# Kernel optimization log

Hardware: AMD Instinct MI355X
Metric: run time of the kernel (lower is better)

The kernel has to match this reference:

```python
import jax, jax.numpy as jnp
import numpy as np

D_MODEL, D_STATE, D_CONV, EXPAND = 384, 16, 4, 2
D_INNER = EXPAND * D_MODEL          # 768
DT_RANK = (D_MODEL + 15) // 16      # 24
BATCH, SEQ = 4, 1024


def setup_inputs() -> dict:
    key = jax.random.key(0)
    ks = jax.random.split(key, 16)
    s = 0.02
    inp = {
        "x": jax.random.normal(ks[0], (BATCH, SEQ, D_MODEL), jnp.float32),
        # LayerNorm
        "ln_g": jnp.ones((D_MODEL,), jnp.float32),
        "ln_b": jnp.zeros((D_MODEL,), jnp.float32),
        # in_proj: d_model -> 2*d_model
        "W_in": jax.random.normal(ks[1], (D_MODEL, 2 * D_MODEL), jnp.float32) * s,
        "b_in": jnp.zeros((2 * D_MODEL,), jnp.float32),
        # SSM: input projection d_model -> d_inner
        "W_si": jax.random.normal(ks[2], (D_MODEL, D_INNER), jnp.float32) * s,
        "b_si": jnp.zeros((D_INNER,), jnp.float32),
        # depthwise causal conv (d_inner, 1, d_conv)
        "conv_w": jax.random.normal(ks[3], (D_INNER, 1, D_CONV), jnp.float32) * s,
        "conv_b": jnp.zeros((D_INNER,), jnp.float32),
        # x_proj: d_inner -> dt_rank + 2*d_state (no bias)
        "W_x": jax.random.normal(ks[4], (D_INNER, DT_RANK + 2 * D_STATE), jnp.float32) * s,
        # dt_proj: dt_rank -> d_inner
        "W_dt": jax.random.normal(ks[5], (DT_RANK, D_INNER), jnp.float32) * s,
        "b_dt": jnp.full((D_INNER,), -4.6, jnp.float32),  # softplus(-4.6) ~ 0.01
        # S4D-real init: A = -exp(A_log)
        "A_log": jnp.broadcast_to(jnp.log(jnp.arange(1, D_STATE + 1, dtype=jnp.float32)), (D_INNER, D_STATE)).copy(),
        "D_skip": jnp.ones((D_INNER,), jnp.float32),
        # SSM output projection d_inner -> d_model
        "W_so": jax.random.normal(ks[6], (D_INNER, D_MODEL), jnp.float32) * s,
        "b_so": jnp.zeros((D_MODEL,), jnp.float32),
        # block out_proj
        "W_out": jax.random.normal(ks[7], (D_MODEL, D_MODEL), jnp.float32) * s,
        "b_out": jnp.zeros((D_MODEL,), jnp.float32),
    }
    return inp


def _silu(v):
    return v * jax.nn.sigmoid(v)


def _selective_ssm(xb, W_si, b_si, conv_w, conv_b, W_x, W_dt, b_dt, A_log, D_skip, W_so, b_so):
    # xb: (B, L, d_model) -> (B, L, d_model)
    u = xb @ W_si + b_si                              # (B,L,Di)
    # causal depthwise conv over L
    uc = jax.lax.conv_general_dilated(
        u.transpose(0, 2, 1), conv_w,
        window_strides=(1,), padding=[(D_CONV - 1, 0)],
        feature_group_count=D_INNER,
        dimension_numbers=("NCH", "OIH", "NCH"))
    u = _silu(uc.transpose(0, 2, 1) + conv_b)          # (B,L,Di)

    x_dbl = u @ W_x                                    # (B,L,dt_rank+2N)
    dtr = x_dbl[..., :DT_RANK]
    Bm = x_dbl[..., DT_RANK:DT_RANK + D_STATE]         # (B,L,N)
    Cm = x_dbl[..., DT_RANK + D_STATE:]                # (B,L,N)
    dt = jax.nn.softplus(dtr @ W_dt + b_dt)            # (B,L,Di)

    A = -jnp.exp(A_log)                                # (Di,N)
    dA = jnp.exp(dt[..., None] * A)                    # (B,L,Di,N)
    dBu = dt[..., None] * Bm[:, :, None, :] * u[..., None]  # (B,L,Di,N)

    def step(h, ts):
        dA_t, dBu_t, C_t = ts                          # (B,Di,N),(B,Di,N),(B,N)
        h = dA_t * h + dBu_t
        y = jnp.einsum("bdn,bn->bd", h, C_t)
        return h, y

    h0 = jnp.zeros((u.shape[0], D_INNER, D_STATE), u.dtype)
    _, ys = jax.lax.scan(step, h0,
                         (dA.transpose(1, 0, 2, 3), dBu.transpose(1, 0, 2, 3), Cm.transpose(1, 0, 2)))
    y = ys.transpose(1, 0, 2) + u * D_skip             # (B,L,Di)
    return y @ W_so + b_so                             # (B,L,d_model)


def reference(x, ln_g, ln_b, W_in, b_in, W_si, b_si, conv_w, conv_b, W_x, W_dt, b_dt,
              A_log, D_skip, W_so, b_so, W_out, b_out):
    residual = x
    mu = jnp.mean(x, axis=-1, keepdims=True)
    var = jnp.var(x, axis=-1, keepdims=True)
    xn = (x - mu) * jax.lax.rsqrt(var + 1e-5) * ln_g + ln_b
    xz = xn @ W_in + b_in
    xb, zb = jnp.split(xz, 2, axis=-1)                 # each (B,L,d_model)

    ssm = lambda v: _selective_ssm(v, W_si, b_si, conv_w, conv_b, W_x, W_dt, b_dt,
                                   A_log, D_skip, W_so, b_so)
    h_fwd = ssm(xb)
    h_bwd = jnp.flip(ssm(jnp.flip(xb, axis=1)), axis=1)

    y = (h_fwd + h_bwd) * _silu(zb)
    out = y @ W_out + b_out
    return residual + out
```

## Files before the change

### kernel.cpp

```cpp
#include <hip/hip_runtime.h>


#define SEQ   1024
#define BATCH 4
#define DM    384
#define DI    768
#define DS    16
#define DTRK  24
#define NX    56
#define ROWS  (BATCH*SEQ)
#define NC    64
#define TC    (SEQ/NC)

#define LOG2E 1.4426950408889634f
#define LN2   0.6931471805599453f

typedef __bf16 bf16;
typedef __attribute__((ext_vector_type(8))) __bf16 bf16x8;
typedef __attribute__((ext_vector_type(4))) float f32x4;

__device__ __forceinline__ float fast_silu(float z) {
    return z * __builtin_amdgcn_rcpf(1.f + __builtin_exp2f(-z * LOG2E));
}
__device__ __forceinline__ float fast_softplus(float v) {
    return (v > 20.f) ? v : __builtin_log2f(1.f + __builtin_exp2f(v * LOG2E)) * LN2;
}

__global__ __launch_bounds__(64) void ln_kernel(
    const float* __restrict__ x, const float* __restrict__ g,
    const float* __restrict__ b, bf16* __restrict__ xn)
{
    int row = blockIdx.x;
    int lane = threadIdx.x;
    const float* xr = x + (size_t)row * DM;
    float v[6]; float s = 0.f, s2 = 0.f;
#pragma unroll
    for (int i = 0; i < 6; ++i) { v[i] = xr[lane + i*64]; s += v[i]; s2 += v[i]*v[i]; }
#pragma unroll
    for (int off = 32; off > 0; off >>= 1) { s += __shfl_down(s, off); s2 += __shfl_down(s2, off); }
    s = __shfl(s, 0); s2 = __shfl(s2, 0);
    float mu = s * (1.f/DM);
    float var = s2 * (1.f/DM) - mu*mu;
    float rs = rsqrtf(var + 1e-5f);
    bf16* xo = xn + (size_t)row * DM;
#pragma unroll
    for (int i = 0; i < 6; ++i) { int c = lane + i*64; xo[c] = (bf16)((v[i]-mu)*rs*g[c] + b[c]); }
}

#define WPE0 294912
#define WPE1 589824
#define WPE2 632832
#define WPE3 927744
#define WPE4 1075200
#define WPTOT (WPE4 + DI*64)
__global__ __launch_bounds__(256) void wprep_kernel(
    const float* __restrict__ W_in, const float* __restrict__ W_si,
    const float* __restrict__ W_x,  const float* __restrict__ W_so,
    const float* __restrict__ W_out, const float* __restrict__ W_dt,
    bf16* __restrict__ wt)
{
    int i = blockIdx.x*256 + threadIdx.x;
    if (i >= WPTOT) return;
    if (i >= WPE4) {
        int j = i - WPE4;
        int n = j >> 6, k = j & 63;
        wt[i] = (k < DTRK) ? (bf16)W_dt[(size_t)k*DI + n] : (bf16)0.f;
        return;
    }
    const float* W; int K, N, base;
    if (i < WPE0)      { W = W_in;  K = 384; N = 768; base = 0; }
    else if (i < WPE1) { W = W_si;  K = 384; N = 768; base = WPE0; }
    else if (i < WPE2) { W = W_x;   K = 768; N = 56;  base = WPE1; }
    else if (i < WPE3) { W = W_so;  K = 768; N = 384; base = WPE2; }
    else               { W = W_out; K = 384; N = 384; base = WPE3; }
    int j = i - base;
    int n = j / K, k = j % K;
    wt[i] = (bf16)W[(size_t)k*N + n];
}

template<int BN>
__global__ __launch_bounds__(256) void gemm_mfma(
    const bf16* __restrict__ A, const bf16* __restrict__ A2, int lda,
    const bf16* __restrict__ Bt,
    const float* __restrict__ bias, float bias_scale,
    float* __restrict__ Cf, int ldcf, int ncut,
    bf16* __restrict__ Cb, int ldcb,
    int M, int N, int K,
    int epi, const float* __restrict__ eptr, int lde)
{
    __shared__ bf16 As[64][72];
    __shared__ bf16 Bs[BN][72];
    const int tid = threadIdx.x;

    int bx = blockIdx.x, by = blockIdx.y;
    {
        int nbx = gridDim.x, nby = gridDim.y;
        if ((nby & 7) == 0) {
            int id = by * nbx + bx;
            int xcd = id & 7, rest = id >> 3;
            int mPerX = nby >> 3;
            by = xcd * mPerX + rest / nbx;
            bx = rest % nbx;
        }
    }
    const int n0 = bx * BN;
    const int m0 = by * 64;
    const int l = tid & 63, w = tid >> 6;
    const int wm = (w >> 1) * 32;
    const int wn = (BN == 64) ? (w & 1) * 32 : (w & 1) * 16;
    const int lm = l & 15, kg = l >> 4;

    const int ar = tid >> 2;
    const int ak = (tid & 3) * 16;

    f32x4 acc[2][BN == 64 ? 2 : 1];
#pragma unroll
    for (int i = 0; i < 2; ++i)
#pragma unroll
        for (int j = 0; j < (BN == 64 ? 2 : 1); ++j) acc[i][j] = (f32x4){0.f,0.f,0.f,0.f};

    for (int k0 = 0; k0 < K; k0 += 64) {
        {
            const bf16* Ab = A + (size_t)(m0+ar)*lda + k0 + ak;
            bf16x8 v0 = *(const bf16x8*)(Ab);
            bf16x8 v1 = *(const bf16x8*)(Ab+8);
            if (A2) {
                const bf16* Ab2 = A2 + (size_t)(m0+ar)*lda + k0 + ak;
                bf16x8 u0 = *(const bf16x8*)(Ab2);
                bf16x8 u1 = *(const bf16x8*)(Ab2+8);
#pragma unroll
                for (int e = 0; e < 8; ++e) {
                    v0[e] = (bf16)((float)v0[e] + (float)u0[e]);
                    v1[e] = (bf16)((float)v1[e] + (float)u1[e]);
                }
            }
            *(bf16x8*)&As[ar][ak]   = v0;
            *(bf16x8*)&As[ar][ak+8] = v1;
        }
        if (BN == 64) {
            int bn = tid >> 2, bk = (tid & 3) * 16;
            int gn = n0 + bn;
            if (gn < N) {
                const bf16* Bp = Bt + (size_t)gn*K + k0 + bk;
                bf16x8 b0 = *(const bf16x8*)(Bp);
                bf16x8 b1 = *(const bf16x8*)(Bp+8);
                *(bf16x8*)&Bs[bn][bk]   = b0;
                *(bf16x8*)&Bs[bn][bk+8] = b1;
            } else {
                bf16x8 z = {};
                *(bf16x8*)&Bs[bn][bk]   = z;
                *(bf16x8*)&Bs[bn][bk+8] = z;
            }
        } else {
            int bn = tid >> 3, bk = (tid & 7) * 8;
            int gn = n0 + bn;
            if (gn < N) {
                *(bf16x8*)&Bs[bn][bk] = *(const bf16x8*)(Bt + (size_t)gn*K + k0 + bk);
            } else {
                bf16x8 z = {};
                *(bf16x8*)&Bs[bn][bk] = z;
            }
        }
        __syncthreads();
#pragma unroll
        for (int kk = 0; kk < 2; ++kk) {
            int co = kk*32 + kg*8;
            bf16x8 a0 = *(const bf16x8*)&As[wm +  0 + lm][co];
            bf16x8 a1 = *(const bf16x8*)&As[wm + 16 + lm][co];
            bf16x8 b0 = *(const bf16x8*)&Bs[wn +  0 + lm][co];
            acc[0][0] = __builtin_amdgcn_mfma_f32_16x16x32_bf16(a0, b0, acc[0][0], 0, 0, 0);
            acc[1][0] = __builtin_amdgcn_mfma_f32_16x16x32_bf16(a1, b0, acc[1][0], 0, 0, 0);
            if (BN == 64) {
                bf16x8 b1 = *(const bf16x8*)&Bs[wn + 16 + lm][co];
                acc[0][BN==64?1:0] = __builtin_amdgcn_mfma_f32_16x16x32_bf16(a0, b1, acc[0][BN==64?1:0], 0, 0, 0);
                acc[1][BN==64?1:0] = __builtin_amdgcn_mfma_f32_16x16x32_bf16(a1, b1, acc[1][BN==64?1:0], 0, 0, 0);
            }
        }
        __syncthreads();
    }

    constexpr int NT = (BN == 64) ? 2 : 1;
    int r0 = kg * 4;
#pragma unroll
    for (int mt = 0; mt < 2; ++mt) {
        int mbase = m0 + wm + mt*16 + r0;
#pragma unroll
        for (int nt = 0; nt < NT; ++nt) {
            int n = n0 + wn + nt*16 + lm;
            if (n >= N) continue;
            float bv = bias ? bias_scale * bias[n] : 0.f;
#pragma unroll
            for (int r = 0; r < 4; ++r) {
                int mm = mbase + r;
                float v = acc[mt][nt][r] + bv;
                if (epi == 1) {
                    v = fast_softplus(v);
                } else if (epi == 2) {
                    v *= fast_silu(eptr[(size_t)mm*lde + n]);
                } else if (epi == 3) {
                    v += eptr[(size_t)mm*lde + n];
                }
                if (Cb) Cb[(size_t)mm*ldcb + n] = (bf16)v;
                if (Cf && n >= ncut) Cf[(size_t)mm*ldcf + (n - ncut)] = v;
            }
        }
    }
}

__global__ __launch_bounds__(256) void conv_silu_kernel(
    const bf16* __restrict__ up, const float* __restrict__ w,
    const float* __restrict__ cb, bf16* __restrict__ uf_bf, bf16* __restrict__ ub_bf)
{
    int i = blockIdx.x * 256 + threadIdx.x;
    if (i >= ROWS*DI) return;
    int d = i % DI;
    int row = i / DI;
    int t = row % SEQ;
    float w0 = w[d*4+0], w1 = w[d*4+1], w2 = w[d*4+2], w3 = w[d*4+3];
    float bias = cb[d];
    const bf16* col = up + (size_t)(row - t) * DI + d;

    float af = bias + (float)col[(size_t)t*DI] * w3;
    if (t >= 1) af += (float)col[(size_t)(t-1)*DI] * w2;
    if (t >= 2) af += (float)col[(size_t)(t-2)*DI] * w1;
    if (t >= 3) af += (float)col[(size_t)(t-3)*DI] * w0;

    float ab = bias + (float)col[(size_t)t*DI] * w3;
    if (t+1 < SEQ) ab += (float)col[(size_t)(t+1)*DI] * w2;
    if (t+2 < SEQ) ab += (float)col[(size_t)(t+2)*DI] * w1;
    if (t+3 < SEQ) ab += (float)col[(size_t)(t+3)*DI] * w0;

    uf_bf[i] = (bf16)fast_silu(af);
    ub_bf[i] = (bf16)fast_silu(ab);
}


__global__ __launch_bounds__(256) void scan_phase_a(
    const bf16* __restrict__ dt, const bf16* __restrict__ u,
    const float* __restrict__ xbc, const float* __restrict__ A_log,
    float* __restrict__ hend, float* __restrict__ sumdt)
{
    int blk = blockIdx.x;
    int dgrp = blk % 3;
    int c = (blk / 3) % NC;
    int dirb = blk / (3*NC);
    int dir = dirb >> 2, b = dirb & 3;
    int d = dgrp * 256 + threadIdx.x;

    size_t base  = ((size_t)dir*ROWS + (size_t)b*SEQ) * DI;
    size_t xbase = ((size_t)dir*ROWS + (size_t)b*SEQ) * 32;

    float c1 = -expf(A_log[d*DS]) * LOG2E;
    float h[DS];
#pragma unroll
    for (int n = 0; n < DS; ++n) h[n] = 0.f;
    float sdt = 0.f;

    for (int s = c*TC; s < (c+1)*TC; ++s) {
        int t = dir ? (SEQ-1-s) : s;
        size_t row = base + (size_t)t * DI;
        float dtv = (float)dt[row + d];
        float uv  = (float)u[row + d];
        sdt += dtv;
        const float* xr = xbc + xbase + (size_t)t * 32;
        float dtu = dtv * uv;
        float r = __builtin_exp2f(dtv * c1);
        float p = 1.f;
#pragma unroll
        for (int n = 0; n < DS; ++n) {
            p *= r;
            h[n] = p * h[n] + xr[n] * dtu;
        }
    }
    size_t cb = (size_t)dirb*NC + c;
    sumdt[cb*DI + d] = sdt;
#pragma unroll
    for (int n = 0; n < DS; ++n)
        hend[(cb*DS + n)*DI + d] = h[n];
}

__global__ __launch_bounds__(256) void scan_phase_b(
    const float* __restrict__ A_log, const float* __restrict__ sumdt,
    float* __restrict__ hstate)
{
    int dirb = blockIdx.x / 48;
    int pair = (blockIdx.x % 48) * 256 + threadIdx.x;
    int n = pair / DI;
    int d = pair % DI;
    float Ac = -expf(A_log[d*DS + n]) * LOG2E;
    float H = 0.f;
    for (int c = 0; c < NC; ++c) {
        size_t cb = (size_t)dirb*NC + c;
        float sdt = sumdt[cb*DI + d];
        size_t idx = (cb*DS + n)*DI + d;
        float he = hstate[idx];
        hstate[idx] = H;
        H = __builtin_exp2f(Ac * sdt) * H + he;
    }
}

__global__ __launch_bounds__(256) void scan_phase_c(
    const bf16* __restrict__ dt, const bf16* __restrict__ u,
    const float* __restrict__ xbc, const float* __restrict__ A_log,
    const float* __restrict__ D_skip, const float* __restrict__ h0,
    bf16* __restrict__ ys)
{
    int blk = blockIdx.x;
    int dgrp = blk % 3;
    int c = (blk / 3) % NC;
    int dirb = blk / (3*NC);
    int dir = dirb >> 2, b = dirb & 3;
    int d = dgrp * 256 + threadIdx.x;

    size_t base  = ((size_t)dir*ROWS + (size_t)b*SEQ) * DI;
    size_t xbase = ((size_t)dir*ROWS + (size_t)b*SEQ) * 32;

    float c1 = -expf(A_log[d*DS]) * LOG2E;
    float h[DS];
    size_t cb = (size_t)dirb*NC + c;
#pragma unroll
    for (int n = 0; n < DS; ++n) h[n] = h0[(cb*DS + n)*DI + d];
    float Dv = D_skip[d];

    for (int s = c*TC; s < (c+1)*TC; ++s) {
        int t = dir ? (SEQ-1-s) : s;
        size_t row = base + (size_t)t * DI;
        float dtv = (float)dt[row + d];
        float uv  = (float)u[row + d];
        const float* xr = xbc + xbase + (size_t)t * 32;
        float dtu = dtv * uv;
        float r = __builtin_exp2f(dtv * c1);
        float p = 1.f;
        float y = 0.f;
#pragma unroll
        for (int n = 0; n < DS; ++n) {
            p *= r;
            h[n] = p * h[n] + xr[n] * dtu;
            y += h[n] * xr[16 + n];
        }
        ys[row + d] = (bf16)(y + uv * Dv);
    }
}

extern "C" void kernel_launch(void* const* d_in, const int* in_sizes, int n_in,
                              void* d_out, int out_size, void* d_ws, size_t ws_size,
                              hipStream_t stream)
{
    const float* x      = (const float*)d_in[0];
    const float* ln_g   = (const float*)d_in[1];
    const float* ln_b   = (const float*)d_in[2];
    const float* W_in   = (const float*)d_in[3];
    const float* b_in   = (const float*)d_in[4];
    const float* W_si   = (const float*)d_in[5];
    const float* b_si   = (const float*)d_in[6];
    const float* conv_w = (const float*)d_in[7];
    const float* conv_b = (const float*)d_in[8];
    const float* W_x    = (const float*)d_in[9];
    const float* W_dt   = (const float*)d_in[10];
    const float* b_dt   = (const float*)d_in[11];
    const float* A_log  = (const float*)d_in[12];
    const float* D_skip = (const float*)d_in[13];
    const float* W_so   = (const float*)d_in[14];
    const float* b_so   = (const float*)d_in[15];
    const float* W_out  = (const float*)d_in[16];
    const float* b_out  = (const float*)d_in[17];
    float* out = (float*)d_out;

    char* wp = (char*)d_ws;
    bf16* xzb    = (bf16*)wp;  wp += (size_t)ROWS*DI*2;
    float* zb    = (float*)wp; wp += (size_t)ROWS*DM*4;
    bf16* xn_bf  = (bf16*)wp;  wp += (size_t)ROWS*DM*2;
    bf16* upreb  = (bf16*)wp;  wp += (size_t)ROWS*DI*2;
    bf16* ucatb  = (bf16*)wp;  wp += (size_t)2*ROWS*DI*2;
    float* xbc   = (float*)wp; wp += (size_t)2*ROWS*32*4;
    bf16* xdblb  = (bf16*)wp;  wp += (size_t)2*ROWS*64*2;
    bf16* dtb    = (bf16*)wp;  wp += (size_t)2*ROWS*DI*2;
    bf16* ysbf   = (bf16*)wp;  wp += (size_t)2*ROWS*DI*2;
    bf16* yb_bf  = (bf16*)wp;  wp += (size_t)ROWS*DM*2;
    bf16* wT     = (bf16*)wp;  wp += (size_t)WPTOT*2;
    float* hend  = (float*)wp; wp += (size_t)8*NC*DS*DI*4;
    float* sumdt = (float*)wp; wp += (size_t)8*NC*DI*4;

    bf16* wt_in  = wT;
    bf16* wt_si  = wT + WPE0;
    bf16* wt_x   = wT + WPE1;
    bf16* wt_so  = wT + WPE2;
    bf16* wt_out = wT + WPE3;
    bf16* wdtp   = wT + WPE4;

    dim3 blk(256);

    wprep_kernel<<<(WPTOT + 255)/256, blk, 0, stream>>>(
        W_in, W_si, W_x, W_so, W_out, W_dt, wT);

    ln_kernel<<<ROWS, 64, 0, stream>>>(x, ln_g, ln_b, xn_bf);

    gemm_mfma<64><<<dim3(12, 64), blk, 0, stream>>>(xn_bf, nullptr, DM, wt_in,
        b_in, 1.f, zb, DM, DM, xzb, 2*DM, ROWS, 2*DM, DM, 0, nullptr, 0);

    gemm_mfma<64><<<dim3(12, 64), blk, 0, stream>>>(xzb, nullptr, 2*DM, wt_si,
        b_si, 1.f, nullptr, 0, 0, upreb, DI, ROWS, DI, DM, 0, nullptr, 0);

    conv_silu_kernel<<<(ROWS*DI + 255)/256, blk, 0, stream>>>(
        upreb, conv_w, conv_b, ucatb, ucatb + (size_t)ROWS*DI);

    gemm_mfma<32><<<dim3(2, 128), blk, 0, stream>>>(ucatb, nullptr, DI, wt_x,
        nullptr, 0.f, xbc, 32, DTRK, xdblb, 64, 2*ROWS, NX, DI, 0, nullptr, 0);

    gemm_mfma<64><<<dim3(12, 128), blk, 0, stream>>>(xdblb, nullptr, 64, wdtp,
        b_dt, 1.f, nullptr, 0, 0, dtb, DI, 2*ROWS, DI, 64, 1, nullptr, 0);

    scan_phase_a<<<8*NC*3, blk, 0, stream>>>(dtb, ucatb, xbc, A_log, hend, sumdt);
    scan_phase_b<<<8*48,   blk, 0, stream>>>(A_log, sumdt, hend);
    scan_phase_c<<<8*NC*3, blk, 0, stream>>>(dtb, ucatb, xbc, A_log, D_skip, hend, ysbf);

    gemm_mfma<32><<<dim3(12, 64), blk, 0, stream>>>(ysbf, ysbf + (size_t)ROWS*DI, DI,
        wt_so, b_so, 2.f, nullptr, 0, 0, yb_bf, DM, ROWS, DM, DI, 2, zb, DM);

    gemm_mfma<32><<<dim3(12, 64), blk, 0, stream>>>(yb_bf, nullptr, DM, wt_out,
        b_out, 1.f, out, DM, 0, nullptr, 0, ROWS, DM, DM, 3, x, DM);
}
```

Measured before the change: 251.5 us.

## Fold in_proj into SSM input projection and fuse LN with weight prep

Precomputes a combined weight W_in[:, :384] @ W_si with a small GEMM, plus a folded bias, so that the z half and the SSM input u come out of a single GEMM from the normalized input (N=1152). The separate in_proj→W_si GEMM chain goes away, and SiLU(z) is applied in that GEMM's epilogue and stored as bf16. LayerNorm, weight transposition and bias folding are merged into one prep kernel, and the conv kernel is vectorized to 8 channels per thread. The cost is an extra weight-folding GEMM and a serial bias loop on each call, plus z gating now reading a bf16 copy, which adds rounding.

```diff
diff --git a/kernel.cpp b/kernel.cpp
--- a/kernel.cpp
+++ b/kernel.cpp
@@ -26,56 +26,82 @@
     return (v > 20.f) ? v : __builtin_log2f(1.f + __builtin_exp2f(v * LOG2E)) * LN2;
 }
 
-__global__ __launch_bounds__(64) void ln_kernel(
-    const float* __restrict__ x, const float* __restrict__ g,
-    const float* __restrict__ b, bf16* __restrict__ xn)
-{
-    int row = blockIdx.x;
-    int lane = threadIdx.x;
-    const float* xr = x + (size_t)row * DM;
-    float v[6]; float s = 0.f, s2 = 0.f;
-#pragma unroll
-    for (int i = 0; i < 6; ++i) { v[i] = xr[lane + i*64]; s += v[i]; s2 += v[i]*v[i]; }
-#pragma unroll
-    for (int off = 32; off > 0; off >>= 1) { s += __shfl_down(s, off); s2 += __shfl_down(s2, off); }
-    s = __shfl(s, 0); s2 = __shfl(s2, 0);
-    float mu = s * (1.f/DM);
-    float var = s2 * (1.f/DM) - mu*mu;
-    float rs = rsqrtf(var + 1e-5f);
-    bf16* xo = xn + (size_t)row * DM;
-#pragma unroll
-    for (int i = 0; i < 6; ++i) { int c = lane + i*64; xo[c] = (bf16)((v[i]-mu)*rs*g[c] + b[c]); }
-}
-
-#define WPE0 294912
-#define WPE1 589824
-#define WPE2 632832
-#define WPE3 927744
-#define WPE4 1075200
-#define WPTOT (WPE4 + DI*64)
-__global__ __launch_bounds__(256) void wprep_kernel(
-    const float* __restrict__ W_in, const float* __restrict__ W_si,
-    const float* __restrict__ W_x,  const float* __restrict__ W_so,
-    const float* __restrict__ W_out, const float* __restrict__ W_dt,
-    bf16* __restrict__ wt)
-{
-    int i = blockIdx.x*256 + threadIdx.x;
-    if (i >= WPTOT) return;
-    if (i >= WPE4) {
-        int j = i - WPE4;
-        int n = j >> 6, k = j & 63;
-        wt[i] = (k < DTRK) ? (bf16)W_dt[(size_t)k*DI + n] : (bf16)0.f;
+#define O_SI   0
+#define O_X    294912
+#define O_SO   337920
+#define O_OUT  632832
+#define O_DTP  780288
+#define O_INNT 829440
+#define WPN    976896
+#define WCTOP  147456
+
+#define LNBLKS 1024
+#define WPBLKS (((WPN + WCTOP) + 255)/256)
+#define BCBLKS 5
+#define PREPGRID (LNBLKS + WPBLKS + BCBLKS)
+
+__global__ __launch_bounds__(256) void prep_kernel(
+    const float* __restrict__ x, const float* __restrict__ ln_g, const float* __restrict__ ln_b,
+    const float* __restrict__ W_in, const float* __restrict__ b_in,
+    const float* __restrict__ W_si, const float* __restrict__ b_si,
+    const float* __restrict__ W_x,  const float* __restrict__ W_dt,
+    const float* __restrict__ W_so, const float* __restrict__ W_out,
+    bf16* __restrict__ xn, bf16* __restrict__ wT, bf16* __restrict__ wcat,
+    float* __restrict__ bcat)
+{
+    int blk = blockIdx.x;
+    int tid = threadIdx.x;
+    if (blk < LNBLKS) {
+        int row = blk*4 + (tid >> 6);
+        int lane = tid & 63;
+        const float* xr = x + (size_t)row * DM;
+        float v[6]; float s = 0.f, s2 = 0.f;
+#pragma unroll
+        for (int i = 0; i < 6; ++i) { v[i] = xr[lane + i*64]; s += v[i]; s2 += v[i]*v[i]; }
+#pragma unroll
+        for (int off = 32; off > 0; off >>= 1) { s += __shfl_down(s, off); s2 += __shfl_down(s2, off); }
+        s = __shfl(s, 0); s2 = __shfl(s2, 0);
+        float mu = s * (1.f/DM);
+        float var = s2 * (1.f/DM) - mu*mu;
+        float rs = rsqrtf(var + 1e-5f);
+        bf16* xo = xn + (size_t)row * DM;
+#pragma unroll
+        for (int i = 0; i < 6; ++i) { int c = lane + i*64; xo[c] = (bf16)((v[i]-mu)*rs*ln_g[c] + ln_b[c]); }
         return;
     }
-    const float* W; int K, N, base;
-    if (i < WPE0)      { W = W_in;  K = 384; N = 768; base = 0; }
-    else if (i < WPE1) { W = W_si;  K = 384; N = 768; base = WPE0; }
-    else if (i < WPE2) { W = W_x;   K = 768; N = 56;  base = WPE1; }
-    else if (i < WPE3) { W = W_so;  K = 768; N = 384; base = WPE2; }
-    else               { W = W_out; K = 384; N = 384; base = WPE3; }
-    int j = i - base;
-    int n = j / K, k = j % K;
-    wt[i] = (bf16)W[(size_t)k*N + n];
+    if (blk < LNBLKS + WPBLKS) {
+        int i = (blk - LNBLKS)*256 + tid;
+        if (i < O_X) {
+            int n = i/384, k = i%384;
+            wT[i] = (bf16)W_si[(size_t)k*768 + n];
+        } else if (i < O_SO) {
+            int j = i - O_X; int n = j/768, k = j%768;
+            wT[i] = (bf16)W_x[(size_t)k*56 + n];
+        } else if (i < O_OUT) {
+            int j = i - O_SO; int n = j/768, k = j%768;
+            wT[i] = (bf16)W_so[(size_t)k*384 + n];
+        } else if (i < O_DTP) {
+            int j = i - O_OUT; int n = j/384, k = j%384;
+            wT[i] = (bf16)W_out[(size_t)k*384 + n];
+        } else if (i < O_INNT) {
+            int j = i - O_DTP; int n = j >> 6, k = j & 63;
+            wT[i] = (k < DTRK) ? (bf16)W_dt[(size_t)k*DI + n] : (bf16)0.f;
+        } else if (i < WPN) {
+            int j2 = i - O_INNT; int j = j2/384, c = j2%384;
+            wT[i] = (bf16)W_in[(size_t)j*768 + c];
+        } else if (i < WPN + WCTOP) {
+            int j2 = i - WPN; int n = j2/384, j = j2%384;
+            wcat[(size_t)n*384 + j] = (bf16)W_in[(size_t)j*768 + 384 + n];
+        }
+        return;
+    }
+    int t = (blk - LNBLKS - WPBLKS)*256 + tid;
+    if (t >= 1152) return;
+    if (t < 384) { bcat[t] = b_in[384 + t]; return; }
+    int n = t - 384;
+    float s = b_si[n];
+    for (int c = 0; c < 384; ++c) s += b_in[c] * W_si[(size_t)c*768 + n];
+    bcat[t] = s;
 }
 
 template<int BN>
@@ -83,10 +109,11 @@
     const bf16* __restrict__ A, const bf16* __restrict__ A2, int lda,
     const bf16* __restrict__ Bt,
     const float* __restrict__ bias, float bias_scale,
-    float* __restrict__ Cf, int ldcf, int ncut,
-    bf16* __restrict__ Cb, int ldcb,
+    float* __restrict__ Cf, int ldcf, int flo, int fhi,
+    bf16* __restrict__ Cb, int ldcb, int blo, int bhi, int transb,
     int M, int N, int K,
-    int epi, const float* __restrict__ eptr, int lde)
+    int epi, int ncut2,
+    const float* __restrict__ epf, const bf16* __restrict__ epb, int lde)
 {
     __shared__ bf16 As[64][72];
     __shared__ bf16 Bs[BN][72];
@@ -195,45 +222,60 @@
                 float v = acc[mt][nt][r] + bv;
                 if (epi == 1) {
                     v = fast_softplus(v);
-                } else if (epi == 2) {
-                    v *= fast_silu(eptr[(size_t)mm*lde + n]);
                 } else if (epi == 3) {
-                    v += eptr[(size_t)mm*lde + n];
+                    v += epf[(size_t)mm*lde + n];
+                } else if (epi == 5) {
+                    v *= (float)epb[(size_t)mm*lde + n];
+                } else if (epi == 6) {
+                    if (n < ncut2) v = fast_silu(v);
                 }
-                if (Cb) Cb[(size_t)mm*ldcb + n] = (bf16)v;
-                if (Cf && n >= ncut) Cf[(size_t)mm*ldcf + (n - ncut)] = v;
+                if (Cb && n >= blo && n < bhi) {
+                    if (transb) Cb[(size_t)(n-blo)*ldcb + mm] = (bf16)v;
+                    else        Cb[(size_t)mm*ldcb + (n-blo)] = (bf16)v;
+                }
+                if (Cf && n >= flo && n < fhi) Cf[(size_t)mm*ldcf + (n-flo)] = v;
             }
         }
     }
 }
 
 __global__ __launch_bounds__(256) void conv_silu_kernel(
-    const bf16* __restrict__ up, const float* __restrict__ w,
-    const float* __restrict__ cb, bf16* __restrict__ uf_bf, bf16* __restrict__ ub_bf)
+    const bf16* __restrict__ zu, const float* __restrict__ w,
+    const float* __restrict__ cb, bf16* __restrict__ uf, bf16* __restrict__ ub)
 {
     int i = blockIdx.x * 256 + threadIdx.x;
-    if (i >= ROWS*DI) return;
-    int d = i % DI;
-    int row = i / DI;
+    if (i >= ROWS*96) return;
+    int dg = i % 96;
+    int row = i / 96;
     int t = row % SEQ;
-    float w0 = w[d*4+0], w1 = w[d*4+1], w2 = w[d*4+2], w3 = w[d*4+3];
-    float bias = cb[d];
-    const bf16* col = up + (size_t)(row - t) * DI + d;
-
-    float af = bias + (float)col[(size_t)t*DI] * w3;
-    if (t >= 1) af += (float)col[(size_t)(t-1)*DI] * w2;
-    if (t >= 2) af += (float)col[(size_t)(t-2)*DI] * w1;
-    if (t >= 3) af += (float)col[(size_t)(t-3)*DI] * w0;
-
-    float ab = bias + (float)col[(size_t)t*DI] * w3;
-    if (t+1 < SEQ) ab += (float)col[(size_t)(t+1)*DI] * w2;
-    if (t+2 < SEQ) ab += (float)col[(size_t)(t+2)*DI] * w1;
-    if (t+3 < SEQ) ab += (float)col[(size_t)(t+3)*DI] * w0;
-
-    uf_bf[i] = (bf16)fast_silu(af);
-    ub_bf[i] = (bf16)fast_silu(ab);
-}
-
+    int bstart = row - t;
+    const bf16* up = zu + 384 + (size_t)dg*8;
+
+    bf16x8 rm3 = {}, rm2 = {}, rm1 = {}, rp1 = {}, rp2 = {}, rp3 = {};
+    bf16x8 r0v = *(const bf16x8*)(up + (size_t)(bstart+t)*1152);
+    if (t >= 1) rm1 = *(const bf16x8*)(up + (size_t)(bstart+t-1)*1152);
+    if (t >= 2) rm2 = *(const bf16x8*)(up + (size_t)(bstart+t-2)*1152);
+    if (t >= 3) rm3 = *(const bf16x8*)(up + (size_t)(bstart+t-3)*1152);
+    if (t+1 < SEQ) rp1 = *(const bf16x8*)(up + (size_t)(bstart+t+1)*1152);
+    if (t+2 < SEQ) rp2 = *(const bf16x8*)(up + (size_t)(bstart+t+2)*1152);
+    if (t+3 < SEQ) rp3 = *(const bf16x8*)(up + (size_t)(bstart+t+3)*1152);
+
+    bf16x8 of, ob;
+#pragma unroll
+    for (int e = 0; e < 8; ++e) {
+        int d = dg*8 + e;
+        float4 wv = *(const float4*)(w + (size_t)d*4);
+        float bias = cb[d];
+        float af = bias + wv.x*(float)rm3[e] + wv.y*(float)rm2[e]
+                        + wv.z*(float)rm1[e] + wv.w*(float)r0v[e];
+        float ab = bias + wv.x*(float)rp3[e] + wv.y*(float)rp2[e]
+                        + wv.z*(float)rp1[e] + wv.w*(float)r0v[e];
+        of[e] = (bf16)fast_silu(af);
+        ob[e] = (bf16)fast_silu(ab);
+    }
+    *(bf16x8*)(uf + (size_t)row*DI + dg*8) = of;
+    *(bf16x8*)(ub + (size_t)row*DI + dg*8) = ob;
+}
 
 __global__ __launch_bounds__(256) void scan_phase_a(
     const bf16* __restrict__ dt, const bf16* __restrict__ u,
@@ -367,56 +409,67 @@
     float* out = (float*)d_out;
 
     char* wp = (char*)d_ws;
-    bf16* xzb    = (bf16*)wp;  wp += (size_t)ROWS*DI*2;
-    float* zb    = (float*)wp; wp += (size_t)ROWS*DM*4;
     bf16* xn_bf  = (bf16*)wp;  wp += (size_t)ROWS*DM*2;
-    bf16* upreb  = (bf16*)wp;  wp += (size_t)ROWS*DI*2;
+    bf16* zu     = (bf16*)wp;  wp += (size_t)ROWS*1152*2;
     bf16* ucatb  = (bf16*)wp;  wp += (size_t)2*ROWS*DI*2;
     float* xbc   = (float*)wp; wp += (size_t)2*ROWS*32*4;
     bf16* xdblb  = (bf16*)wp;  wp += (size_t)2*ROWS*64*2;
     bf16* dtb    = (bf16*)wp;  wp += (size_t)2*ROWS*DI*2;
     bf16* ysbf   = (bf16*)wp;  wp += (size_t)2*ROWS*DI*2;
     bf16* yb_bf  = (bf16*)wp;  wp += (size_t)ROWS*DM*2;
-    bf16* wT     = (bf16*)wp;  wp += (size_t)WPTOT*2;
+    bf16* wT     = (bf16*)wp;  wp += (size_t)WPN*2;
+    bf16* wcat   = (bf16*)wp;  wp += (size_t)1152*384*2;
+    float* bcat  = (float*)wp; wp += (size_t)1152*4;
     float* hend  = (float*)wp; wp += (size_t)8*NC*DS*DI*4;
     float* sumdt = (float*)wp; wp += (size_t)8*NC*DI*4;
 
-    bf16* wt_in  = wT;
-    bf16* wt_si  = wT + WPE0;
-    bf16* wt_x   = wT + WPE1;
-    bf16* wt_so  = wT + WPE2;
-    bf16* wt_out = wT + WPE3;
-    bf16* wdtp   = wT + WPE4;
+    bf16* wt_si  = wT + O_SI;
+    bf16* wt_x   = wT + O_X;
+    bf16* wt_so  = wT + O_SO;
+    bf16* wt_out = wT + O_OUT;
+    bf16* wdtp   = wT + O_DTP;
+    bf16* win_nt = wT + O_INNT;
 
     dim3 blk(256);
 
-    wprep_kernel<<<(WPTOT + 255)/256, blk, 0, stream>>>(
-        W_in, W_si, W_x, W_so, W_out, W_dt, wT);
-
-    ln_kernel<<<ROWS, 64, 0, stream>>>(x, ln_g, ln_b, xn_bf);
-
-    gemm_mfma<64><<<dim3(12, 64), blk, 0, stream>>>(xn_bf, nullptr, DM, wt_in,
-        b_in, 1.f, zb, DM, DM, xzb, 2*DM, ROWS, 2*DM, DM, 0, nullptr, 0);
-
-    gemm_mfma<64><<<dim3(12, 64), blk, 0, stream>>>(xzb, nullptr, 2*DM, wt_si,
-        b_si, 1.f, nullptr, 0, 0, upreb, DI, ROWS, DI, DM, 0, nullptr, 0);
-
-    conv_silu_kernel<<<(ROWS*DI + 255)/256, blk, 0, stream>>>(
-        upreb, conv_w, conv_b, ucatb, ucatb + (size_t)ROWS*DI);
-
-    gemm_mfma<32><<<dim3(2, 128), blk, 0, stream>>>(ucatb, nullptr, DI, wt_x,
-        nullptr, 0.f, xbc, 32, DTRK, xdblb, 64, 2*ROWS, NX, DI, 0, nullptr, 0);
-
-    gemm_mfma<64><<<dim3(12, 128), blk, 0, stream>>>(xdblb, nullptr, 64, wdtp,
-        b_dt, 1.f, nullptr, 0, 0, dtb, DI, 2*ROWS, DI, 64, 1, nullptr, 0);
+    prep_kernel<<<PREPGRID, blk, 0, stream>>>(
+        x, ln_g, ln_b, W_in, b_in, W_si, b_si, W_x, W_dt, W_so, W_out,
+        xn_bf, wT, wcat, bcat);
+
+    gemm_mfma<64><<<dim3(12, 6), blk, 0, stream>>>(
+        win_nt, nullptr, 384, wt_si, nullptr, 0.f,
+        nullptr, 0, 0, 0, wcat + (size_t)384*384, 384, 0, 768, 1,
+        384, 768, 384, 0, 0, nullptr, nullptr, 0);
+
+    gemm_mfma<64><<<dim3(18, 64), blk, 0, stream>>>(
+        xn_bf, nullptr, DM, wcat, bcat, 1.f,
+        nullptr, 0, 0, 0, zu, 1152, 0, 1152, 0,
+        ROWS, 1152, DM, 6, 384, nullptr, nullptr, 0);
+
+    conv_silu_kernel<<<(ROWS*96 + 255)/256, blk, 0, stream>>>(
+        zu, conv_w, conv_b, ucatb, ucatb + (size_t)ROWS*DI);
+
+    gemm_mfma<32><<<dim3(2, 128), blk, 0, stream>>>(
+        ucatb, nullptr, DI, wt_x, nullptr, 0.f,
+        xbc, 32, DTRK, NX, xdblb, 64, 0, NX, 0,
+        2*ROWS, NX, DI, 0, 0, nullptr, nullptr, 0);
+
+    gemm_mfma<64><<<dim3(12, 128), blk, 0, stream>>>(
+        xdblb, nullptr, 64, wdtp, b_dt, 1.f,
+        nullptr, 0, 0, 0, dtb, DI, 0, DI, 0,
+        2*ROWS, DI, 64, 1, 0, nullptr, nullptr, 0);
 
     scan_phase_a<<<8*NC*3, blk, 0, stream>>>(dtb, ucatb, xbc, A_log, hend, sumdt);
     scan_phase_b<<<8*48,   blk, 0, stream>>>(A_log, sumdt, hend);
     scan_phase_c<<<8*NC*3, blk, 0, stream>>>(dtb, ucatb, xbc, A_log, D_skip, hend, ysbf);
 
-    gemm_mfma<32><<<dim3(12, 64), blk, 0, stream>>>(ysbf, ysbf + (size_t)ROWS*DI, DI,
-        wt_so, b_so, 2.f, nullptr, 0, 0, yb_bf, DM, ROWS, DM, DI, 2, zb, DM);
-
-    gemm_mfma<32><<<dim3(12, 64), blk, 0, stream>>>(yb_bf, nullptr, DM, wt_out,
-        b_out, 1.f, out, DM, 0, nullptr, 0, ROWS, DM, DM, 3, x, DM);
-}
+    gemm_mfma<32><<<dim3(12, 64), blk, 0, stream>>>(
+        ysbf, ysbf + (size_t)ROWS*DI, DI, wt_so, b_so, 2.f,
+        nullptr, 0, 0, 0, yb_bf, DM, 0, DM, 0,
+        ROWS, DM, DI, 5, 0, nullptr, zu, 1152);
+
+    gemm_mfma<32><<<dim3(12, 64), blk, 0, stream>>>(
+        yb_bf, nullptr, DM, wt_out, b_out, 1.f,
+        out, DM, 0, DM, nullptr, 0, 0, 0, 0,
+        ROWS, DM, DM, 3, 0, x, nullptr, DM);
+}
```

New measurement: 264.4 us. +5.1%, slower.
